# Kernel optimization log

Hardware: AMD Instinct MI355X
Metric: run time of the kernel (lower is better)

Reference implementation:

```python
import jax, jax.numpy as jnp
import numpy as np

SEQ, BATCH, IN, HS = 512, 64, 512, 1024
FORGET_BIAS = 0.0

def setup_inputs() -> dict:
    key = jax.random.key(0)
    ks = jax.random.split(key, 6)
    stdv = 1.0 / np.sqrt(HS)
    u = lambda k, shape: jax.random.uniform(k, shape, jnp.float32, -stdv, stdv)
    return {
        "x": jax.random.normal(ks[0], (SEQ, BATCH, IN), jnp.float32),
        "W": u(ks[1], (IN + HS, 4 * HS)),
        "bias": u(ks[2], (4 * HS,)),
        "peep_i": u(ks[3], (HS,)),
        "peep_f": u(ks[4], (HS,)),
        "peep_o": u(ks[5], (HS,)),
    }

def reference(x, W, bias, peep_i, peep_f, peep_o):
    bs = x.shape[1]
    c0 = jnp.zeros((bs, HS), x.dtype)
    h0 = jnp.zeros((bs, HS), x.dtype)

    def step(carry, x_t):
        c, h = carry
        # gates: [B, 4H] = [x_t | h] @ W + bias
        gates = jnp.concatenate([x_t, h], axis=1) @ W + bias
        i_t, j_t, f_t, o_t = jnp.split(gates, 4, axis=1)
        c_new = (jax.nn.sigmoid(f_t + FORGET_BIAS + c * peep_f) * c
                 + jax.nn.sigmoid(i_t + c * peep_i) * jnp.tanh(j_t))
        h_new = jax.nn.sigmoid(o_t + c_new * peep_o) * jnp.tanh(c_new)
        return (c_new, h_new), h_new

    (c_T, h_T), hidden_seq = jax.lax.scan(step, (c0, h0), x)
    return hidden_seq, (c_T, h_T)
```

## Files before the change

kernel.cpp:

```cpp
#include <hip/hip_runtime.h>
#include <hip/hip_bf16.h>


#define SEQN 512
#define BATCH 64
#define INDIM 512
#define HSZ 1024
#define NWG 128
#define DEPTH 64

typedef __attribute__((ext_vector_type(8))) short s16x8;
typedef __attribute__((ext_vector_type(4))) float f32x4;
typedef __attribute__((ext_vector_type(2))) float f32x2;
typedef __attribute__((ext_vector_type(4))) int i32x4;
typedef unsigned long long u64;

__device__ __forceinline__ short f2bf(float f) {
  __hip_bfloat16 b = __float2bfloat16(f);
  short s;
  __builtin_memcpy(&s, &b, 2);
  return s;
}
__device__ __forceinline__ float sigf(float x) { return 1.f / (1.f + __expf(-x)); }
__device__ __forceinline__ float tanh_fast(float x) { return 2.f / (1.f + __expf(-2.f * x)) - 1.f; }

__global__ __launch_bounds__(256) void prep_w(const float* __restrict__ W,
                                              short* __restrict__ WxP,
                                              short* __restrict__ WhP) {
  int idx = blockIdx.x * 256 + threadIdx.x;
  if (idx >= 1536 * 4096) return;
  int k = idx >> 12, col = idx & 4095;
  short b = f2bf(W[idx]);
  int gate = col >> 10, hidx = col & 1023;
  int g = hidx >> 3, off = hidx & 7;
  int pc = off * 4 + gate;
  if (k < 512) {
    WxP[(size_t)(((g * 64 + (k >> 3)) * 32 + pc) << 3) + (k & 7)] = b;
  } else {
    int kh = k - 512;
    WhP[(size_t)(((g * 128 + (kh >> 3)) * 32 + pc) << 3) + (kh & 7)] = b;
  }
}

__global__ __launch_bounds__(256) void prep_x(const float* __restrict__ x,
                                              short* __restrict__ xbp) {
  int idx = blockIdx.x * 256 + threadIdx.x;
  if (idx >= SEQN * 64 * 64) return;
  int kb = idx & 63, m = (idx >> 6) & 63, t = idx >> 12;
  const float4* xp = reinterpret_cast<const float4*>(x + ((size_t)t * 64 + m) * 512 + kb * 8);
  float4 a = xp[0], c = xp[1];
  s16x8 v;
  v[0] = f2bf(a.x); v[1] = f2bf(a.y); v[2] = f2bf(a.z); v[3] = f2bf(a.w);
  v[4] = f2bf(c.x); v[5] = f2bf(c.y); v[6] = f2bf(c.z); v[7] = f2bf(c.w);
  reinterpret_cast<s16x8*>(xbp)[((size_t)t * 64 + kb) * 64 + m] = v;
}

__global__ __launch_bounds__(256, 1) void lstm_seq(const short* __restrict__ xbp,
                                                   const short* __restrict__ WhP,
                                                   const short* __restrict__ WxP,
                                                   const float* __restrict__ bias,
                                                   const float* __restrict__ peep_i,
                                                   const float* __restrict__ peep_f,
                                                   const float* __restrict__ peep_o,
                                                   u64* hqt,
                                                   float* __restrict__ out) {
  __shared__ short WhS[32768];
  __shared__ short WxS[16384];
  __shared__ float outS[512];
  int g = blockIdx.x;
  int tid = threadIdx.x, w = tid >> 6, l = tid & 63;
  {
    const s16x8* src = reinterpret_cast<const s16x8*>(WhP + (size_t)g * 32768);
    s16x8* dst = reinterpret_cast<s16x8*>(WhS);
#pragma unroll
    for (int i = 0; i < 16; ++i) dst[i * 256 + tid] = src[i * 256 + tid];
    const s16x8* src2 = reinterpret_cast<const s16x8*>(WxP + (size_t)g * 16384);
    s16x8* dst2 = reinterpret_cast<s16x8*>(WxS);
#pragma unroll
    for (int i = 0; i < 8; ++i) dst2[i * 256 + tid] = src2[i * 256 + tid];
  }
  int m = w * 16 + (l & 15), q4 = l >> 4, l15 = l & 15;
  int c0 = g * 8 + q4, c1 = c0 + 4;
  float bi0 = bias[c0], bj0 = bias[1024 + c0], bf0 = bias[2048 + c0], bo0 = bias[3072 + c0];
  float bi1 = bias[c1], bj1 = bias[1024 + c1], bf1 = bias[2048 + c1], bo1 = bias[3072 + c1];
  float pi0 = peep_i[c0], pf0 = peep_f[c0], po0 = peep_o[c0];
  float pi1 = peep_i[c1], pf1 = peep_f[c1], po1 = peep_o[c1];
  float cr0 = 0.f, cr1 = 0.f;
  s16x8* WhS16 = reinterpret_cast<s16x8*>(WhS);
  s16x8* WxS16 = reinterpret_cast<s16x8*>(WxS);
  __syncthreads();

#define LOADG(BANK, G)                                                                   \
  {                                                                                      \
    _Pragma("unroll") for (int i = 0; i < 16; ++i) {                                     \
      int kb_ = ((G) * 8 + (i >> 1)) * 4 + q4;                                           \
      BANK[i] = *reinterpret_cast<const i32x4*>(rdq + kb_ * 256 + m * 4 + (i & 1) * 2);  \
    }                                                                                    \
  }
#define RELOADG(BANK, G)                                                                 \
  {                                                                                      \
    _Pragma("unroll") for (int i = 0; i < 16; ++i) {                                     \
      int kb_ = ((G) * 8 + (i >> 1)) * 4 + q4;                                           \
      const u64* p_ = rdq + kb_ * 256 + m * 4 + (i & 1) * 2;                             \
      asm volatile("global_load_dwordx4 %0, %1, off sc0 sc1" : "=v"(BANK[i]) : "v"(p_)); \
    }                                                                                    \
    asm volatile("s_waitcnt vmcnt(0)" ::: "memory");                                     \
    __builtin_amdgcn_sched_barrier(0);                                                   \
  }
#define CHECKG(BANK, G)                                                                  \
  {                                                                                      \
    int guard = 0;                                                                       \
    while (true) {                                                                       \
      bool ok = true;                                                                    \
      _Pragma("unroll") for (int i = 0; i < 16; ++i) ok &=                               \
          ((unsigned)BANK[i][1] == (unsigned)t) & ((unsigned)BANK[i][3] == (unsigned)t); \
      if (__all((int)ok)) break;                                                         \
      if (++guard > (1 << 13)) break;                         \
      RELOADG(BANK, G);                                                                  \
    }                                                                                    \
  }
#define MFMAG(BANK, G)                                                                   \
  {                                                                                      \
    _Pragma("unroll") for (int kk2 = 0; kk2 < 8; ++kk2) {                                \
      int kb_ = ((G) * 8 + kk2) * 4 + q4;                                                \
      unsigned d0 = (unsigned)BANK[kk2 * 2][0], d1 = (unsigned)BANK[kk2 * 2][2];         \
      unsigned d2 = (unsigned)BANK[kk2 * 2 + 1][0], d3 = (unsigned)BANK[kk2 * 2 + 1][2]; \
      union { unsigned u[4]; s16x8 v; } bu;                                              \
      bu.u[0] = (d0 & 0xFFFFu) | (d1 << 16);                                             \
      bu.u[1] = (d2 & 0xFFFFu) | (d3 << 16);                                             \
      bu.u[2] = (d0 >> 16) | (d1 & 0xFFFF0000u);                                         \
      bu.u[3] = (d2 >> 16) | (d3 & 0xFFFF0000u);                                        \
      s16x8 a0 = WhS16[kb_ * 32 + l15];                                                  \
      s16x8 a1 = WhS16[kb_ * 32 + 16 + l15];                                             \
      acc0 = __builtin_amdgcn_mfma_f32_16x16x32_bf16(a0, bu.v, acc0, 0, 0, 0);           \
      acc1 = __builtin_amdgcn_mfma_f32_16x16x32_bf16(a1, bu.v, acc1, 0, 0, 0);           \
    }                                                                                    \
  }

  for (int t = 0; t < SEQN; ++t) {
    f32x4 acc0 = {0.f, 0.f, 0.f, 0.f}, acc1 = {0.f, 0.f, 0.f, 0.f};
    {
      const s16x8* xt = reinterpret_cast<const s16x8*>(xbp) + (size_t)t * 4096;
#pragma unroll 4
      for (int kk = 0; kk < 16; ++kk) {
        int kb = kk * 4 + q4;
        s16x8 bx = xt[kb * 64 + m];
        s16x8 a0 = WxS16[kb * 32 + l15];
        s16x8 a1 = WxS16[kb * 32 + 16 + l15];
        acc0 = __builtin_amdgcn_mfma_f32_16x16x32_bf16(a0, bx, acc0, 0, 0, 0);
        acc1 = __builtin_amdgcn_mfma_f32_16x16x32_bf16(a1, bx, acc1, 0, 0, 0);
      }
    }
    if (t > 0) {
      const u64* rdq = hqt + (size_t)(t & (DEPTH - 1)) * 32768;
      i32x4 hA[16], hB[16];
      LOADG(hA, 0);
      LOADG(hB, 1);
      CHECKG(hA, 0);
      MFMAG(hA, 0);
      LOADG(hA, 2);
      CHECKG(hB, 1);
      MFMAG(hB, 1);
      LOADG(hB, 3);
      CHECKG(hA, 2);
      MFMAG(hA, 2);
      CHECKG(hB, 3);
      MFMAG(hB, 3);
    }
    float i0 = sigf(acc0[0] + bi0 + cr0 * pi0);
    float f0 = sigf(acc0[2] + bf0 + cr0 * pf0);
    float cn0 = f0 * cr0 + i0 * tanh_fast(acc0[1] + bj0);
    float o0 = sigf(acc0[3] + bo0 + cn0 * po0);
    float h0 = o0 * tanh_fast(cn0);
    cr0 = cn0;
    float i1 = sigf(acc1[0] + bi1 + cr1 * pi1);
    float f1 = sigf(acc1[2] + bf1 + cr1 * pf1);
    float cn1 = f1 * cr1 + i1 * tanh_fast(acc1[1] + bj1);
    float o1 = sigf(acc1[3] + bo1 + cn1 * po1);
    float h1 = o1 * tanh_fast(cn1);
    cr1 = cn1;
    {
      u64 q = ((u64)(unsigned)(t + 1) << 32) |
              ((u64)(unsigned short)f2bf(h1) << 16) | (u64)(unsigned short)f2bf(h0);
      (void)__hip_atomic_exchange(
          hqt + (size_t)((t + 1) & (DEPTH - 1)) * 32768 + g * 256 + m * 4 + q4, q,
          __ATOMIC_RELAXED, __HIP_MEMORY_SCOPE_AGENT);
    }
    outS[w * 128 + l15 * 8 + q4] = h0;
    outS[w * 128 + l15 * 8 + q4 + 4] = h1;
    {
      f32x2 v = *reinterpret_cast<f32x2*>(&outS[w * 128 + (l >> 2) * 8 + (l & 3) * 2]);
      int row = w * 16 + (l >> 2), col = g * 8 + (l & 3) * 2;
      __builtin_nontemporal_store(
          v, reinterpret_cast<f32x2*>(out + (size_t)t * 65536 + (size_t)row * 1024 + col));
    }
    if (t == SEQN - 1) {
      out[33554432ull + (size_t)m * 1024 + c0] = cn0;
      out[33554432ull + (size_t)m * 1024 + c1] = cn1;
      out[33619968ull + (size_t)m * 1024 + c0] = h0;
      out[33619968ull + (size_t)m * 1024 + c1] = h1;
    }
  }
#undef LOADG
#undef RELOADG
#undef CHECKG
#undef MFMAG
}

extern "C" void kernel_launch(void* const* d_in, const int* in_sizes, int n_in,
                              void* d_out, int out_size, void* d_ws, size_t ws_size,
                              hipStream_t stream) {
  const float* x      = (const float*)d_in[0];
  const float* W      = (const float*)d_in[1];
  const float* bias   = (const float*)d_in[2];
  const float* peep_i = (const float*)d_in[3];
  const float* peep_f = (const float*)d_in[4];
  const float* peep_o = (const float*)d_in[5];
  char* ws = (char*)d_ws;
  short* WxP = (short*)(ws);
  short* WhP = (short*)(ws + 4194304ull);
  short* xbp = (short*)(ws + 12582912ull);
  u64* hqt   = (u64*)(ws + 46137344ull);
  (void)hipMemsetAsync(hqt, 0, 16777216ull, stream);
  prep_w<<<24576, 256, 0, stream>>>(W, WxP, WhP);
  prep_x<<<8192, 256, 0, stream>>>(x, xbp);
  lstm_seq<<<NWG, 256, 0, stream>>>(xbp, WhP, WxP, bias, peep_i, peep_f, peep_o, hqt,
                                    (float*)d_out);
}
```

Before: 2.587 ms.

## Relay hidden state through per-cluster staging buffers for local reads

Workgroups are grouped into clusters of eight (g&7). Each workgroup copies one slice of the step's hidden-state queue into a cluster-private staging buffer, then reads its full h input from that buffer with sc0 (not sc0 sc1) loads. The goal is to cut cross-die coherent traffic and polling on the global queue, presumably by keeping data in a closer cache domain. This adds a spin-poll, a block-wide barrier and an extra copy on every step. It also adds a fallback to the old path if tag checks keep failing, but the staging buffer is never zeroed, so stale tags could collide with the step index.

Measured after the change: 3.690 ms. +42.7%, slower.

```diff
diff --git a/kernel.cpp b/kernel.cpp
--- a/kernel.cpp
+++ b/kernel.cpp
@@ -8,6 +8,7 @@
 #define HSZ 1024
 #define NWG 128
 #define DEPTH 64
+#define SDEPTH 8
 
 typedef __attribute__((ext_vector_type(8))) short s16x8;
 typedef __attribute__((ext_vector_type(4))) float f32x4;
@@ -63,12 +64,16 @@
                                                    const float* __restrict__ peep_f,
                                                    const float* __restrict__ peep_o,
                                                    u64* hqt,
+                                                   u64* stg,
                                                    float* __restrict__ out) {
   __shared__ short WhS[32768];
   __shared__ short WxS[16384];
   __shared__ float outS[512];
+  __shared__ int fbS;
   int g = blockIdx.x;
   int tid = threadIdx.x, w = tid >> 6, l = tid & 63;
+  int cluster = g & 7, crank = g >> 3;
+  u64* stgc = stg + (size_t)cluster * (SDEPTH * 32768);
   {
     const s16x8* src = reinterpret_cast<const s16x8*>(WhP + (size_t)g * 32768);
     s16x8* dst = reinterpret_cast<s16x8*>(WhS);
@@ -79,6 +84,7 @@
 #pragma unroll
     for (int i = 0; i < 8; ++i) dst2[i * 256 + tid] = src2[i * 256 + tid];
   }
+  if (tid == 0) fbS = 0;
   int m = w * 16 + (l & 15), q4 = l >> 4, l15 = l & 15;
   int c0 = g * 8 + q4, c1 = c0 + 4;
   float bi0 = bias[c0], bj0 = bias[1024 + c0], bf0 = bias[2048 + c0], bo0 = bias[3072 + c0];
@@ -86,16 +92,34 @@
   float pi0 = peep_i[c0], pf0 = peep_f[c0], po0 = peep_o[c0];
   float pi1 = peep_i[c1], pf1 = peep_f[c1], po1 = peep_o[c1];
   float cr0 = 0.f, cr1 = 0.f;
+  int relayok = 1, fellback = 0;
   s16x8* WhS16 = reinterpret_cast<s16x8*>(WhS);
   s16x8* WxS16 = reinterpret_cast<s16x8*>(WxS);
   __syncthreads();
 
+#define TAGTEST(BANK)                                                                    \
+  {                                                                                      \
+    okv = true;                                                                          \
+    _Pragma("unroll") for (int i2 = 0; i2 < 16; ++i2) okv &=                             \
+        ((unsigned)BANK[i2][1] == (unsigned)t) & ((unsigned)BANK[i2][3] == (unsigned)t); \
+  }
 #define LOADG(BANK, G)                                                                   \
   {                                                                                      \
+    const u64* fdq_ = relayok ? sdq : rdq;                                               \
     _Pragma("unroll") for (int i = 0; i < 16; ++i) {                                     \
       int kb_ = ((G) * 8 + (i >> 1)) * 4 + q4;                                           \
-      BANK[i] = *reinterpret_cast<const i32x4*>(rdq + kb_ * 256 + m * 4 + (i & 1) * 2);  \
-    }                                                                                    \
+      BANK[i] = *reinterpret_cast<const i32x4*>(fdq_ + kb_ * 256 + m * 4 + (i & 1) * 2); \
+    }                                                                                    \
+  }
+#define SLOADG(BANK, G)                                                                  \
+  {                                                                                      \
+    _Pragma("unroll") for (int i = 0; i < 16; ++i) {                                     \
+      int kb_ = ((G) * 8 + (i >> 1)) * 4 + q4;                                           \
+      const u64* p_ = sdq + kb_ * 256 + m * 4 + (i & 1) * 2;                             \
+      asm volatile("global_load_dwordx4 %0, %1, off sc0" : "=v"(BANK[i]) : "v"(p_));     \
+    }                                                                                    \
+    asm volatile("s_waitcnt vmcnt(0)" ::: "memory");                                     \
+    __builtin_amdgcn_sched_barrier(0);                                                   \
   }
 #define RELOADG(BANK, G)                                                                 \
   {                                                                                      \
@@ -109,14 +133,22 @@
   }
 #define CHECKG(BANK, G)                                                                  \
   {                                                                                      \
-    int guard = 0;                                                                       \
-    while (true) {                                                                       \
-      bool ok = true;                                                                    \
-      _Pragma("unroll") for (int i = 0; i < 16; ++i) ok &=                               \
-          ((unsigned)BANK[i][1] == (unsigned)t) & ((unsigned)BANK[i][3] == (unsigned)t); \
-      if (__all((int)ok)) break;                                                         \
-      if (++guard > (1 << 13)) break;                         \
-      RELOADG(BANK, G);                                                                  \
+    bool okv;                                                                            \
+    TAGTEST(BANK);                                                                       \
+    int rr = 0;                                                                          \
+    while (relayok && !__all((int)okv) && rr < 4) {                                      \
+      SLOADG(BANK, G);                                                                   \
+      TAGTEST(BANK);                                                                     \
+      ++rr;                                                                              \
+    }                                                                                    \
+    if (!__all((int)okv)) {                                                              \
+      if (t >= 4) ++fellback;                                                            \
+      int guard = 0;                                                                     \
+      while (!__all((int)okv)) {                                                         \
+        RELOADG(BANK, G);                                                                \
+        TAGTEST(BANK);                                                                   \
+        if (++guard > (1 << 13)) break;                       \
+      }                                                                                  \
     }                                                                                    \
   }
 #define MFMAG(BANK, G)                                                                   \
@@ -153,6 +185,31 @@
     }
     if (t > 0) {
       const u64* rdq = hqt + (size_t)(t & (DEPTH - 1)) * 32768;
+      const u64* sdq = stgc + (size_t)(t & (SDEPTH - 1)) * 32768;
+      if (relayok) {
+        const u64* rsrc = rdq + crank * 2048 + tid * 8;
+        u64* rdst = const_cast<u64*>(sdq) + crank * 2048 + tid * 8;
+        i32x4 rv[4];
+        int guard = 0;
+        while (true) {
+#pragma unroll
+          for (int i = 0; i < 4; ++i) {
+            const u64* p_ = rsrc + i * 2;
+            asm volatile("global_load_dwordx4 %0, %1, off sc0 sc1" : "=v"(rv[i]) : "v"(p_));
+          }
+          asm volatile("s_waitcnt vmcnt(0)" ::: "memory");
+          __builtin_amdgcn_sched_barrier(0);
+          bool ok = true;
+#pragma unroll
+          for (int i = 0; i < 4; ++i)
+            ok &= ((unsigned)rv[i][1] == (unsigned)t) & ((unsigned)rv[i][3] == (unsigned)t);
+          if (__all((int)ok)) break;
+          if (++guard > (1 << 13)) break;
+        }
+#pragma unroll
+        for (int i = 0; i < 4; ++i) *reinterpret_cast<i32x4*>(rdst + i * 2) = rv[i];
+        __syncthreads();
+      }
       i32x4 hA[16], hB[16];
       LOADG(hA, 0);
       LOADG(hB, 1);
@@ -200,8 +257,15 @@
       out[33619968ull + (size_t)m * 1024 + c0] = h0;
       out[33619968ull + (size_t)m * 1024 + c1] = h1;
     }
-  }
+    if (t == 8) {
+      if (l == 0) atomicAdd(&fbS, fellback);
+      __syncthreads();
+      if (fbS > 16) relayok = 0;
+    }
+  }
+#undef TAGTEST
 #undef LOADG
+#undef SLOADG
 #undef RELOADG
 #undef CHECKG
 #undef MFMAG
@@ -221,9 +285,10 @@
   short* WhP = (short*)(ws + 4194304ull);
   short* xbp = (short*)(ws + 12582912ull);
   u64* hqt   = (u64*)(ws + 46137344ull);
+  u64* stg   = (u64*)(ws + 62914560ull);
   (void)hipMemsetAsync(hqt, 0, 16777216ull, stream);
   prep_w<<<24576, 256, 0, stream>>>(W, WxP, WhP);
   prep_x<<<8192, 256, 0, stream>>>(x, xbp);
-  lstm_seq<<<NWG, 256, 0, stream>>>(xbp, WhP, WxP, bias, peep_i, peep_f, peep_o, hqt,
+  lstm_seq<<<NWG, 256, 0, stream>>>(xbp, WhP, WxP, bias, peep_i, peep_f, peep_o, hqt, stg,
                                     (float*)d_out);
 }
```

## Add per-workgroup gate flags polled before loading the hidden-state queue

Applied to the files above, without the earlier changes.

Before reading the previous step's hidden state, each wavefront now polls a compact array of per-workgroup flags, one per producer workgroup, and only then runs the tagged h loads and checks. Each producer workgroup counts its four waves' finished writes in a shared-memory counter, and the last wave publishes a step flag. The ring depth is cut from 64 to 16 and the memset shrinks to match. The aim is cheaper cross-workgroup synchronisation through polling a small region instead of spinning on the large tagged h buffer. The cost is an extra vmcnt(0) wait and an atomic on every step, plus a spin guard that silently breaks out after a fixed count.

Measured after the change: 3.031 ms. 17.2% more time.

```diff
diff --git a/kernel.cpp b/kernel.cpp
--- a/kernel.cpp
+++ b/kernel.cpp
@@ -7,7 +7,7 @@
 #define INDIM 512
 #define HSZ 1024
 #define NWG 128
-#define DEPTH 64
+#define DEPTH 16
 
 typedef __attribute__((ext_vector_type(8))) short s16x8;
 typedef __attribute__((ext_vector_type(4))) float f32x4;
@@ -63,10 +63,12 @@
                                                    const float* __restrict__ peep_f,
                                                    const float* __restrict__ peep_o,
                                                    u64* hqt,
+                                                   u64* gates,
                                                    float* __restrict__ out) {
   __shared__ short WhS[32768];
   __shared__ short WxS[16384];
   __shared__ float outS[512];
+  __shared__ unsigned ctrS;
   int g = blockIdx.x;
   int tid = threadIdx.x, w = tid >> 6, l = tid & 63;
   {
@@ -79,6 +81,7 @@
 #pragma unroll
     for (int i = 0; i < 8; ++i) dst2[i * 256 + tid] = src2[i * 256 + tid];
   }
+  if (tid == 0) ctrS = 0;
   int m = w * 16 + (l & 15), q4 = l >> 4, l15 = l & 15;
   int c0 = g * 8 + q4, c1 = c0 + 4;
   float bi0 = bias[c0], bj0 = bias[1024 + c0], bf0 = bias[2048 + c0], bo0 = bias[3072 + c0];
@@ -153,6 +156,22 @@
     }
     if (t > 0) {
       const u64* rdq = hqt + (size_t)(t & (DEPTH - 1)) * 32768;
+      {
+        const u64* gq = gates + (size_t)(t & (DEPTH - 1)) * 1024;
+        const u64* p0 = gq + (size_t)(2 * l) * 8;
+        const u64* p1 = gq + (size_t)(2 * l + 1) * 8;
+        int guard = 0;
+        while (true) {
+          u64 v0, v1;
+          asm volatile("global_load_dwordx2 %0, %1, off sc0 sc1" : "=v"(v0) : "v"(p0));
+          asm volatile("global_load_dwordx2 %0, %1, off sc0 sc1" : "=v"(v1) : "v"(p1));
+          asm volatile("s_waitcnt vmcnt(0)" ::: "memory");
+          __builtin_amdgcn_sched_barrier(0);
+          if (__all((int)((v0 == (u64)(unsigned)t) & (v1 == (u64)(unsigned)t)))) break;
+          if (++guard > (1 << 15)) break;
+          __builtin_amdgcn_s_sleep(2);
+        }
+      }
       i32x4 hA[16], hB[16];
       LOADG(hA, 0);
       LOADG(hB, 1);
@@ -186,6 +205,15 @@
           hqt + (size_t)((t + 1) & (DEPTH - 1)) * 32768 + g * 256 + m * 4 + q4, q,
           __ATOMIC_RELAXED, __HIP_MEMORY_SCOPE_AGENT);
     }
+    asm volatile("s_waitcnt vmcnt(0)" ::: "memory");
+    if (l == 0) {
+      unsigned old = atomicAdd(&ctrS, 1u);
+      if (old == 4u * (unsigned)t + 3u) {
+        (void)__hip_atomic_exchange(
+            gates + (size_t)((t + 1) & (DEPTH - 1)) * 1024 + (size_t)g * 8,
+            (u64)(unsigned)(t + 1), __ATOMIC_RELAXED, __HIP_MEMORY_SCOPE_AGENT);
+      }
+    }
     outS[w * 128 + l15 * 8 + q4] = h0;
     outS[w * 128 + l15 * 8 + q4 + 4] = h1;
     {
@@ -221,9 +249,10 @@
   short* WhP = (short*)(ws + 4194304ull);
   short* xbp = (short*)(ws + 12582912ull);
   u64* hqt   = (u64*)(ws + 46137344ull);
-  (void)hipMemsetAsync(hqt, 0, 16777216ull, stream);
+  u64* gates = (u64*)(ws + 50331648ull);
+  (void)hipMemsetAsync(hqt, 0, 4325376ull, stream);
   prep_w<<<24576, 256, 0, stream>>>(W, WxP, WhP);
   prep_x<<<8192, 256, 0, stream>>>(x, xbp);
   lstm_seq<<<NWG, 256, 0, stream>>>(xbp, WhP, WxP, bias, peep_i, peep_f, peep_o, hqt,
-                                    (float*)d_out);
-}
+                                    gates, (float*)d_out);
+}
```

## Add per-workgroup readiness flags polled before loading hidden-state chunks

Applied to the files above, without the earlier changes.

Adds a gate-flag array in which each workgroup publishes a single step counter once all four of its wavefronts have written their h values. Before each group load, consumers spin on the 32 producer flags for that group, sleeping between polls. The aim is to replace retries on the large tagged h loads with cheap polling on small flags. The cost is extra atomics, a vmcnt wait on the critical path, and a guarded spin that breaks out after a timeout without ensuring the data is ready.

New measurement: 3.339 ms. +29.1%, slower.

```diff
diff --git a/kernel.cpp b/kernel.cpp
--- a/kernel.cpp
+++ b/kernel.cpp
@@ -63,10 +63,12 @@
                                                    const float* __restrict__ peep_f,
                                                    const float* __restrict__ peep_o,
                                                    u64* hqt,
+                                                   u64* gates,
                                                    float* __restrict__ out) {
   __shared__ short WhS[32768];
   __shared__ short WxS[16384];
   __shared__ float outS[512];
+  __shared__ unsigned ctrS;
   int g = blockIdx.x;
   int tid = threadIdx.x, w = tid >> 6, l = tid & 63;
   {
@@ -79,6 +81,7 @@
 #pragma unroll
     for (int i = 0; i < 8; ++i) dst2[i * 256 + tid] = src2[i * 256 + tid];
   }
+  if (tid == 0) ctrS = 0;
   int m = w * 16 + (l & 15), q4 = l >> 4, l15 = l & 15;
   int c0 = g * 8 + q4, c1 = c0 + 4;
   float bi0 = bias[c0], bj0 = bias[1024 + c0], bf0 = bias[2048 + c0], bo0 = bias[3072 + c0];
@@ -90,6 +93,20 @@
   s16x8* WxS16 = reinterpret_cast<s16x8*>(WxS);
   __syncthreads();
 
+#define GATEW(G)                                                                         \
+  {                                                                                      \
+    const u64* gp_ = gq + (size_t)((G) * 32 + (l & 31)) * 8;                             \
+    int guard = 0;                                                                       \
+    while (true) {                                                                       \
+      u64 v_;                                                                            \
+      asm volatile("global_load_dwordx2 %0, %1, off sc0 sc1" : "=v"(v_) : "v"(gp_));     \
+      asm volatile("s_waitcnt vmcnt(0)" ::: "memory");                                   \
+      __builtin_amdgcn_sched_barrier(0);                                                 \
+      if (__all((int)(v_ == (u64)(unsigned)t))) break;                                   \
+      if (++guard > (1 << 15)) break;     \
+      __builtin_amdgcn_s_sleep(1);                                                       \
+    }                                                                                    \
+  }
 #define LOADG(BANK, G)                                                                   \
   {                                                                                      \
     _Pragma("unroll") for (int i = 0; i < 16; ++i) {                                     \
@@ -153,14 +170,19 @@
     }
     if (t > 0) {
       const u64* rdq = hqt + (size_t)(t & (DEPTH - 1)) * 32768;
+      const u64* gq = gates + (size_t)(t & (DEPTH - 1)) * 1024;
       i32x4 hA[16], hB[16];
+      GATEW(0);
       LOADG(hA, 0);
+      GATEW(1);
       LOADG(hB, 1);
       CHECKG(hA, 0);
       MFMAG(hA, 0);
+      GATEW(2);
       LOADG(hA, 2);
       CHECKG(hB, 1);
       MFMAG(hB, 1);
+      GATEW(3);
       LOADG(hB, 3);
       CHECKG(hA, 2);
       MFMAG(hA, 2);
@@ -186,6 +208,15 @@
           hqt + (size_t)((t + 1) & (DEPTH - 1)) * 32768 + g * 256 + m * 4 + q4, q,
           __ATOMIC_RELAXED, __HIP_MEMORY_SCOPE_AGENT);
     }
+    asm volatile("s_waitcnt vmcnt(0)" ::: "memory");
+    if (l == 0) {
+      unsigned old = atomicAdd(&ctrS, 1u);
+      if (old == 4u * (unsigned)t + 3u) {
+        (void)__hip_atomic_exchange(
+            gates + (size_t)((t + 1) & (DEPTH - 1)) * 1024 + (size_t)g * 8,
+            (u64)(unsigned)(t + 1), __ATOMIC_RELAXED, __HIP_MEMORY_SCOPE_AGENT);
+      }
+    }
     outS[w * 128 + l15 * 8 + q4] = h0;
     outS[w * 128 + l15 * 8 + q4 + 4] = h1;
     {
@@ -201,6 +232,7 @@
       out[33619968ull + (size_t)m * 1024 + c1] = h1;
     }
   }
+#undef GATEW
 #undef LOADG
 #undef RELOADG
 #undef CHECKG
@@ -221,9 +253,10 @@
   short* WhP = (short*)(ws + 4194304ull);
   short* xbp = (short*)(ws + 12582912ull);
   u64* hqt   = (u64*)(ws + 46137344ull);
-  (void)hipMemsetAsync(hqt, 0, 16777216ull, stream);
+  u64* gates = (u64*)(ws + 62914560ull);
+  (void)hipMemsetAsync(hqt, 0, 17301504ull, stream);
   prep_w<<<24576, 256, 0, stream>>>(W, WxP, WhP);
   prep_x<<<8192, 256, 0, stream>>>(x, xbp);
   lstm_seq<<<NWG, 256, 0, stream>>>(xbp, WhP, WxP, bias, peep_i, peep_f, peep_o, hqt,
-                                    (float*)d_out);
-}
+                                    gates, (float*)d_out);
+}
```
